# Kernel optimization log

Measured on AMD Instinct MI355X. Metric: run time of the kernel, lower is better.

Reference implementation:

```python
import jax, jax.numpy as jnp
import numpy as np

NEG_INF = -1e12
BN_EPS = 1e-5
ALPHA = 0.2  # LeakyReLU negative slope


def setup_inputs() -> dict:
    key = jax.random.key(0)
    k1, k2, k3, k4 = jax.random.split(key, 4)
    N, Fin, Fout = 8192, 128, 64
    inp = jax.random.normal(k1, (N, Fin), dtype=jnp.float32)
    adj = jax.random.randint(k2, (N, N), 0, 2, dtype=jnp.int32)
    W = jax.random.normal(k3, (Fin, Fout), dtype=jnp.float32) * (1.414 / np.sqrt(Fin))
    a = jax.random.normal(k4, (2 * Fout, 1), dtype=jnp.float32) * 0.1
    bn_gamma = jnp.ones((Fout,), dtype=jnp.float32)
    bn_beta = jnp.zeros((Fout,), dtype=jnp.float32)
    bn_mean = jnp.zeros((Fout,), dtype=jnp.float32)
    bn_var = jnp.ones((Fout,), dtype=jnp.float32)
    return {"inp": inp, "adj": adj, "W": W, "a": a,
            "bn_gamma": bn_gamma, "bn_beta": bn_beta,
            "bn_mean": bn_mean, "bn_var": bn_var}


def reference(inp, adj, W, a, bn_gamma, bn_beta, bn_mean, bn_var):
    # h: [N, Fout]
    h = inp @ W
    Fout = h.shape[1]
    # Split 'a' into the two halves acting on h_i and h_j:
    # e_ij = leakyrelu(a1 . h_i + a2 . h_j)  (math-equivalent to the
    # O(N^2 * 2F) repeat/cat construction in the original code)
    a1 = a[:Fout, 0]  # [Fout]
    a2 = a[Fout:, 0]  # [Fout]
    f1 = h @ a1       # [N]
    f2 = h @ a2       # [N]
    e = jax.nn.leaky_relu(f1[:, None] + f2[None, :], negative_slope=ALPHA)  # [N, N]
    e = jnp.where(adj > 0, e, NEG_INF)
    attention = jax.nn.softmax(e, axis=1)  # row-wise softmax over neighbors
    # dropout is identity in eval mode
    h_prime = attention @ h  # [N, Fout]
    # BatchNorm1d in eval mode with running stats
    h_prime = (h_prime - bn_mean) * jax.lax.rsqrt(bn_var + BN_EPS) * bn_gamma + bn_beta
    return jax.nn.elu(h_prime)  # concat=True -> ELU
```

## Files before the change

### kernel.cpp

```cpp
#include <hip/hip_runtime.h>
#include <hip/hip_bf16.h>

#define LRALPHA 0.2f
#define NN 8192
#define FIN 128
#define FOUT 64
#define TI 16
#define TJ 128
#define NT (NN / TJ)

typedef __attribute__((ext_vector_type(4))) float f32x4;
typedef __attribute__((ext_vector_type(8))) short bf16x8;
typedef __attribute__((ext_vector_type(4))) int int4v;

__device__ __forceinline__ void barrier_lgkm() {
  asm volatile("s_waitcnt lgkmcnt(0)\n\ts_barrier" ::: "memory");
}

__global__ __launch_bounds__(256) void prep_kernel(
    const float* __restrict__ inp, const float* __restrict__ Wg,
    const float* __restrict__ ag, float* __restrict__ f1,
    float* __restrict__ f2, unsigned short* __restrict__ hT)
{
  __shared__ alignas(16) float WlT[FOUT][FIN + 4];
  const int t = threadIdx.x;
  for (int i = t; i < FIN * FOUT; i += 256)
    WlT[i & 63][i >> 6] = Wg[i];
  __syncthreads();

  const int lane = t & 63;
  const int row0 = blockIdx.x * 16 + (t >> 6) * 4;

  float h0 = 0.f, h1 = 0.f, h2 = 0.f, h3 = 0.f;
  for (int kk = 0; kk < FIN; kk += 4) {
    f32x4 wv = *(const f32x4*)&WlT[lane][kk];
    f32x4 r0 = *(const f32x4*)&inp[(row0 + 0) * FIN + kk];
    f32x4 r1 = *(const f32x4*)&inp[(row0 + 1) * FIN + kk];
    f32x4 r2 = *(const f32x4*)&inp[(row0 + 2) * FIN + kk];
    f32x4 r3 = *(const f32x4*)&inp[(row0 + 3) * FIN + kk];
    h0 += r0[0]*wv[0] + r0[1]*wv[1] + r0[2]*wv[2] + r0[3]*wv[3];
    h1 += r1[0]*wv[0] + r1[1]*wv[1] + r1[2]*wv[2] + r1[3]*wv[3];
    h2 += r2[0]*wv[0] + r2[1]*wv[1] + r2[2]*wv[2] + r2[3]*wv[3];
    h3 += r3[0]*wv[0] + r3[1]*wv[1] + r3[2]*wv[2] + r3[3]*wv[3];
  }

  const float a1v = ag[lane], a2v = ag[64 + lane];
  float hv[4] = {h0, h1, h2, h3};
#pragma unroll
  for (int rr = 0; rr < 4; ++rr) {
    float c1 = hv[rr] * a1v;
    float c2 = hv[rr] * a2v;
#pragma unroll
    for (int off = 32; off > 0; off >>= 1) {
      c1 += __shfl_xor(c1, off);
      c2 += __shfl_xor(c2, off);
    }
    if (lane == 0) { f1[row0 + rr] = c1; f2[row0 + rr] = c2; }
    __hip_bfloat16 hb = __float2bfloat16(hv[rr]);
    hT[lane * NN + row0 + rr] = __builtin_bit_cast(unsigned short, hb);
  }
}

__global__ __launch_bounds__(256) void f2max_kernel(
    const float* __restrict__ f2, float* __restrict__ f2m)
{
  const int t = threadIdx.x;
  float m = -1e30f;
  for (int i = t; i < NN / 4; i += 256) {
    f32x4 v = ((const f32x4*)f2)[i];
    m = fmaxf(fmaxf(m, fmaxf(v[0], v[1])), fmaxf(v[2], v[3]));
  }
#pragma unroll
  for (int off = 32; off > 0; off >>= 1)
    m = fmaxf(m, __shfl_xor(m, off));
  __shared__ float ms[4];
  if ((t & 63) == 0) ms[t >> 6] = m;
  __syncthreads();
  if (t == 0)
    f2m[0] = fmaxf(fmaxf(ms[0], ms[1]), fmaxf(ms[2], ms[3]));
}

__global__ __launch_bounds__(256, 2) void gat_main(
    const int* __restrict__ adj, const float* __restrict__ f1g,
    const float* __restrict__ f2g, const float* __restrict__ f2m,
    const unsigned short* __restrict__ hTg,
    const float* __restrict__ bng, const float* __restrict__ bnb,
    const float* __restrict__ bnm, const float* __restrict__ bnv,
    float* __restrict__ out)
{
  __shared__ alignas(16) unsigned short Pl[TI][TJ + 8];
  __shared__ alignas(16) unsigned short Hl[FOUT][TJ + 8];

  const int t = threadIdx.x;
  const int i0 = blockIdx.x * TI;

  const int pr = t >> 4;
  const int pj = (t & 15) << 3;

  const float f1v = f1g[i0 + pr];
  const float fmv = f2m[0];
  float mrow = f1v + fmv;
  mrow = mrow > 0.f ? mrow : LRALPHA * mrow;

  const int hc = t >> 2;
  const int hj = (t & 3) << 5;

  const int* adjrow = adj + (i0 + pr) * NN + pj;
  const unsigned short* hrow = hTg + hc * NN + hj;
  const float* f2row = f2g + pj;

  f32x4 acc  = {0.f, 0.f, 0.f, 0.f};
  f32x4 accs = {0.f, 0.f, 0.f, 0.f};

  const short ob = (short)0x3F80;
  const bf16x8 onesv = {ob, ob, ob, ob, ob, ob, ob, ob};

  int4v aA0 = __builtin_nontemporal_load((const int4v*)adjrow);
  int4v aA1 = __builtin_nontemporal_load((const int4v*)(adjrow + 4));
  f32x4 fA0 = *(const f32x4*)f2row;
  f32x4 fA1 = *(const f32x4*)(f2row + 4);
  int4v hA0 = *(const int4v*)hrow;
  int4v hA1 = *(const int4v*)(hrow + 8);
  int4v hA2 = *(const int4v*)(hrow + 16);
  int4v hA3 = *(const int4v*)(hrow + 24);

  int4v aB0 = __builtin_nontemporal_load((const int4v*)(adjrow + TJ));
  int4v aB1 = __builtin_nontemporal_load((const int4v*)(adjrow + TJ + 4));
  f32x4 fB0 = *(const f32x4*)(f2row + TJ);
  f32x4 fB1 = *(const f32x4*)(f2row + TJ + 4);
  int4v hB0 = *(const int4v*)(hrow + TJ);
  int4v hB1 = *(const int4v*)(hrow + TJ + 8);
  int4v hB2 = *(const int4v*)(hrow + TJ + 16);
  int4v hB3 = *(const int4v*)(hrow + TJ + 24);

  const int l = t & 63;
  const int w = t >> 6;
  const int koff = (l >> 4) << 3;
  const unsigned short* pA = &Pl[l & 15][koff];
  const unsigned short* pB = &Hl[(w << 4) + (l & 15)][koff];

#define TILE_BODY(TT, AJ0, AJ1, F20, F21, H0, H1, H2, H3)                      \
  {                                                                            \
    float x0 = f1v + F20[0]; x0 = (x0 > 0.f ? x0 : LRALPHA * x0) - mrow;       \
    float x1 = f1v + F20[1]; x1 = (x1 > 0.f ? x1 : LRALPHA * x1) - mrow;       \
    float x2 = f1v + F20[2]; x2 = (x2 > 0.f ? x2 : LRALPHA * x2) - mrow;       \
    float x3 = f1v + F20[3]; x3 = (x3 > 0.f ? x3 : LRALPHA * x3) - mrow;       \
    float x4 = f1v + F21[0]; x4 = (x4 > 0.f ? x4 : LRALPHA * x4) - mrow;       \
    float x5 = f1v + F21[1]; x5 = (x5 > 0.f ? x5 : LRALPHA * x5) - mrow;       \
    float x6 = f1v + F21[2]; x6 = (x6 > 0.f ? x6 : LRALPHA * x6) - mrow;       \
    float x7 = f1v + F21[3]; x7 = (x7 > 0.f ? x7 : LRALPHA * x7) - mrow;       \
    float p0 = AJ0[0] > 0 ? __expf(x0) : 0.f;                                  \
    float p1 = AJ0[1] > 0 ? __expf(x1) : 0.f;                                  \
    float p2 = AJ0[2] > 0 ? __expf(x2) : 0.f;                                  \
    float p3 = AJ0[3] > 0 ? __expf(x3) : 0.f;                                  \
    float p4 = AJ1[0] > 0 ? __expf(x4) : 0.f;                                  \
    float p5 = AJ1[1] > 0 ? __expf(x5) : 0.f;                                  \
    float p6 = AJ1[2] > 0 ? __expf(x6) : 0.f;                                  \
    float p7 = AJ1[3] > 0 ? __expf(x7) : 0.f;                                  \
    unsigned short u0 = __builtin_bit_cast(unsigned short, __float2bfloat16(p0)); \
    unsigned short u1 = __builtin_bit_cast(unsigned short, __float2bfloat16(p1)); \
    unsigned short u2 = __builtin_bit_cast(unsigned short, __float2bfloat16(p2)); \
    unsigned short u3 = __builtin_bit_cast(unsigned short, __float2bfloat16(p3)); \
    unsigned short u4 = __builtin_bit_cast(unsigned short, __float2bfloat16(p4)); \
    unsigned short u5 = __builtin_bit_cast(unsigned short, __float2bfloat16(p5)); \
    unsigned short u6 = __builtin_bit_cast(unsigned short, __float2bfloat16(p6)); \
    unsigned short u7 = __builtin_bit_cast(unsigned short, __float2bfloat16(p7)); \
    int4v pw = {(int)u0 | ((int)u1 << 16), (int)u2 | ((int)u3 << 16),          \
                (int)u4 | ((int)u5 << 16), (int)u6 | ((int)u7 << 16)};         \
    *(int4v*)&Pl[pr][pj] = pw;                                                 \
    *(int4v*)&Hl[hc][hj]      = H0;                                            \
    *(int4v*)&Hl[hc][hj + 8]  = H1;                                            \
    *(int4v*)&Hl[hc][hj + 16] = H2;                                            \
    *(int4v*)&Hl[hc][hj + 24] = H3;                                            \
    if ((TT) + 2 < NT) {                                                       \
      AJ0 = __builtin_nontemporal_load((const int4v*)(adjrow + ((TT)+2)*TJ));      \
      AJ1 = __builtin_nontemporal_load((const int4v*)(adjrow + ((TT)+2)*TJ + 4));  \
      F20 = *(const f32x4*)(f2row + ((TT)+2)*TJ);                              \
      F21 = *(const f32x4*)(f2row + ((TT)+2)*TJ + 4);                          \
      H0 = *(const int4v*)(hrow + ((TT)+2)*TJ);                                \
      H1 = *(const int4v*)(hrow + ((TT)+2)*TJ + 8);                            \
      H2 = *(const int4v*)(hrow + ((TT)+2)*TJ + 16);                           \
      H3 = *(const int4v*)(hrow + ((TT)+2)*TJ + 24);                           \
    }                                                                          \
    barrier_lgkm();                                                            \
    {                                                                          \
      bf16x8 av, bv;                                                           \
      av = *(const bf16x8*)(pA);       bv = *(const bf16x8*)(pB);              \
      acc  = __builtin_amdgcn_mfma_f32_16x16x32_bf16(av, bv, acc, 0, 0, 0);    \
      accs = __builtin_amdgcn_mfma_f32_16x16x32_bf16(av, onesv, accs, 0, 0, 0);\
      av = *(const bf16x8*)(pA + 32);  bv = *(const bf16x8*)(pB + 32);         \
      acc  = __builtin_amdgcn_mfma_f32_16x16x32_bf16(av, bv, acc, 0, 0, 0);    \
      accs = __builtin_amdgcn_mfma_f32_16x16x32_bf16(av, onesv, accs, 0, 0, 0);\
      av = *(const bf16x8*)(pA + 64);  bv = *(const bf16x8*)(pB + 64);         \
      acc  = __builtin_amdgcn_mfma_f32_16x16x32_bf16(av, bv, acc, 0, 0, 0);    \
      accs = __builtin_amdgcn_mfma_f32_16x16x32_bf16(av, onesv, accs, 0, 0, 0);\
      av = *(const bf16x8*)(pA + 96);  bv = *(const bf16x8*)(pB + 96);         \
      acc  = __builtin_amdgcn_mfma_f32_16x16x32_bf16(av, bv, acc, 0, 0, 0);    \
      accs = __builtin_amdgcn_mfma_f32_16x16x32_bf16(av, onesv, accs, 0, 0, 0);\
    }                                                                          \
    barrier_lgkm();                                                            \
  }

  for (int tt = 0; tt < NT; tt += 2) {
    TILE_BODY(tt,     aA0, aA1, fA0, fA1, hA0, hA1, hA2, hA3);
    TILE_BODY(tt + 1, aB0, aB1, fB0, fB1, hB0, hB1, hB2, hB3);
  }
#undef TILE_BODY

  const int gcol = (w << 4) + (l & 15);
  const float inv_sd = rsqrtf(bnv[gcol] + 1e-5f);
  const float ga = bng[gcol], be = bnb[gcol], mu = bnm[gcol];
  const int rbase = (l >> 4) << 2;
#pragma unroll
  for (int q = 0; q < 4; ++q) {
    float v = acc[q] / accs[q];
    v = (v - mu) * inv_sd * ga + be;
    v = v > 0.f ? v : expm1f(v);
    out[(i0 + rbase + q) * FOUT + gcol] = v;
  }
}

extern "C" void kernel_launch(void* const* d_in, const int* in_sizes, int n_in,
                              void* d_out, int out_size, void* d_ws, size_t ws_size,
                              hipStream_t stream)
{
  (void)in_sizes; (void)n_in; (void)out_size; (void)ws_size;
  const float* inp = (const float*)d_in[0];
  const int*   adj = (const int*)d_in[1];
  const float* Wg  = (const float*)d_in[2];
  const float* ag  = (const float*)d_in[3];
  const float* bng = (const float*)d_in[4];
  const float* bnb = (const float*)d_in[5];
  const float* bnm = (const float*)d_in[6];
  const float* bnv = (const float*)d_in[7];
  float* out = (float*)d_out;

  char* ws = (char*)d_ws;
  unsigned short* hT = (unsigned short*)ws;
  float* f1 = (float*)(ws + (size_t)NN * FOUT * 2);
  float* f2 = f1 + NN;
  float* f2m = f2 + NN;

  prep_kernel<<<NN / 16, 256, 0, stream>>>(inp, Wg, ag, f1, f2, hT);
  f2max_kernel<<<1, 256, 0, stream>>>(f2, f2m);
  gat_main<<<NN / TI, 256, 0, stream>>>(adj, f1, f2, f2m, hT,
                                        bng, bnb, bnm, bnv, out);
}
```

Measured before the change: 105.3 us.

## Deepen prefetch to four tiles and compute softmax row sums in fp32

Raises the register prefetch depth from two to four tiles of adjacency, f2 and hT data, to hide more global-memory latency. Drops the extra MFMA that multiplied P by a ones vector to get the denominator. Each thread now accumulates the row sum in fp32 and reduces it with shuffles and shared memory. Adjacency loads are split into two 16-byte halves at offsets 0 and 64, and LeakyReLU uses fmaxf. The deeper prefetch costs more VGPRs, which may hurt occupancy under launch_bounds(256,2), and past the end it reloads the last tile redundantly.

```diff
diff --git a/kernel.cpp b/kernel.cpp
--- a/kernel.cpp
+++ b/kernel.cpp
@@ -12,6 +12,7 @@
 typedef __attribute__((ext_vector_type(4))) float f32x4;
 typedef __attribute__((ext_vector_type(8))) short bf16x8;
 typedef __attribute__((ext_vector_type(4))) int int4v;
+typedef __attribute__((ext_vector_type(2))) int int2v;
 
 __device__ __forceinline__ void barrier_lgkm() {
   asm volatile("s_waitcnt lgkmcnt(0)\n\ts_barrier" ::: "memory");
@@ -90,12 +91,13 @@
 {
   __shared__ alignas(16) unsigned short Pl[TI][TJ + 8];
   __shared__ alignas(16) unsigned short Hl[FOUT][TJ + 8];
+  __shared__ float rs_lds[TI];
 
   const int t = threadIdx.x;
   const int i0 = blockIdx.x * TI;
 
   const int pr = t >> 4;
-  const int pj = (t & 15) << 3;
+  const int c  = t & 15;
 
   const float f1v = f1g[i0 + pr];
   const float fmv = f2m[0];
@@ -105,33 +107,12 @@
   const int hc = t >> 2;
   const int hj = (t & 3) << 5;
 
-  const int* adjrow = adj + (i0 + pr) * NN + pj;
+  const int* adjrow = adj + (i0 + pr) * NN + c * 4;
   const unsigned short* hrow = hTg + hc * NN + hj;
-  const float* f2row = f2g + pj;
-
-  f32x4 acc  = {0.f, 0.f, 0.f, 0.f};
-  f32x4 accs = {0.f, 0.f, 0.f, 0.f};
-
-  const short ob = (short)0x3F80;
-  const bf16x8 onesv = {ob, ob, ob, ob, ob, ob, ob, ob};
-
-  int4v aA0 = __builtin_nontemporal_load((const int4v*)adjrow);
-  int4v aA1 = __builtin_nontemporal_load((const int4v*)(adjrow + 4));
-  f32x4 fA0 = *(const f32x4*)f2row;
-  f32x4 fA1 = *(const f32x4*)(f2row + 4);
-  int4v hA0 = *(const int4v*)hrow;
-  int4v hA1 = *(const int4v*)(hrow + 8);
-  int4v hA2 = *(const int4v*)(hrow + 16);
-  int4v hA3 = *(const int4v*)(hrow + 24);
-
-  int4v aB0 = __builtin_nontemporal_load((const int4v*)(adjrow + TJ));
-  int4v aB1 = __builtin_nontemporal_load((const int4v*)(adjrow + TJ + 4));
-  f32x4 fB0 = *(const f32x4*)(f2row + TJ);
-  f32x4 fB1 = *(const f32x4*)(f2row + TJ + 4);
-  int4v hB0 = *(const int4v*)(hrow + TJ);
-  int4v hB1 = *(const int4v*)(hrow + TJ + 8);
-  int4v hB2 = *(const int4v*)(hrow + TJ + 16);
-  int4v hB3 = *(const int4v*)(hrow + TJ + 24);
+  const float* f2row = f2g + c * 4;
+
+  f32x4 acc = {0.f, 0.f, 0.f, 0.f};
+  float rs = 0.f;
 
   const int l = t & 63;
   const int w = t >> 6;
@@ -139,24 +120,48 @@
   const unsigned short* pA = &Pl[l & 15][koff];
   const unsigned short* pB = &Hl[(w << 4) + (l & 15)][koff];
 
-#define TILE_BODY(TT, AJ0, AJ1, F20, F21, H0, H1, H2, H3)                      \
+  int4v aA0,aA1,aB0,aB1,aC0,aC1,aD0,aD1;
+  f32x4 fA0,fA1,fB0,fB1,fC0,fC1,fD0,fD1;
+  int4v hA0,hA1,hA2,hA3,hB0,hB1,hB2,hB3;
+  int4v hC0,hC1,hC2,hC3,hD0,hD1,hD2,hD3;
+
+#define PREF(A0,A1,F0,F1,H0,H1,H2,H3,T)                                        \
   {                                                                            \
-    float x0 = f1v + F20[0]; x0 = (x0 > 0.f ? x0 : LRALPHA * x0) - mrow;       \
-    float x1 = f1v + F20[1]; x1 = (x1 > 0.f ? x1 : LRALPHA * x1) - mrow;       \
-    float x2 = f1v + F20[2]; x2 = (x2 > 0.f ? x2 : LRALPHA * x2) - mrow;       \
-    float x3 = f1v + F20[3]; x3 = (x3 > 0.f ? x3 : LRALPHA * x3) - mrow;       \
-    float x4 = f1v + F21[0]; x4 = (x4 > 0.f ? x4 : LRALPHA * x4) - mrow;       \
-    float x5 = f1v + F21[1]; x5 = (x5 > 0.f ? x5 : LRALPHA * x5) - mrow;       \
-    float x6 = f1v + F21[2]; x6 = (x6 > 0.f ? x6 : LRALPHA * x6) - mrow;       \
-    float x7 = f1v + F21[3]; x7 = (x7 > 0.f ? x7 : LRALPHA * x7) - mrow;       \
-    float p0 = AJ0[0] > 0 ? __expf(x0) : 0.f;                                  \
-    float p1 = AJ0[1] > 0 ? __expf(x1) : 0.f;                                  \
-    float p2 = AJ0[2] > 0 ? __expf(x2) : 0.f;                                  \
-    float p3 = AJ0[3] > 0 ? __expf(x3) : 0.f;                                  \
-    float p4 = AJ1[0] > 0 ? __expf(x4) : 0.f;                                  \
-    float p5 = AJ1[1] > 0 ? __expf(x5) : 0.f;                                  \
-    float p6 = AJ1[2] > 0 ? __expf(x6) : 0.f;                                  \
-    float p7 = AJ1[3] > 0 ? __expf(x7) : 0.f;                                  \
+    const int _tn = (T) < NT ? (T) : (NT - 1);                                 \
+    A0 = __builtin_nontemporal_load((const int4v*)(adjrow + _tn * TJ));        \
+    A1 = __builtin_nontemporal_load((const int4v*)(adjrow + _tn * TJ + 64));   \
+    F0 = *(const f32x4*)(f2row + _tn * TJ);                                    \
+    F1 = *(const f32x4*)(f2row + _tn * TJ + 64);                               \
+    H0 = *(const int4v*)(hrow + _tn * TJ);                                     \
+    H1 = *(const int4v*)(hrow + _tn * TJ + 8);                                 \
+    H2 = *(const int4v*)(hrow + _tn * TJ + 16);                                \
+    H3 = *(const int4v*)(hrow + _tn * TJ + 24);                                \
+  }
+
+  PREF(aA0,aA1,fA0,fA1,hA0,hA1,hA2,hA3, 0);
+  PREF(aB0,aB1,fB0,fB1,hB0,hB1,hB2,hB3, 1);
+  PREF(aC0,aC1,fC0,fC1,hC0,hC1,hC2,hC3, 2);
+  PREF(aD0,aD1,fD0,fD1,hD0,hD1,hD2,hD3, 3);
+
+#define TILE_BODY(A0,A1,F0,F1,H0,H1,H2,H3,T)                                   \
+  {                                                                            \
+    float x0 = f1v + F0[0]; x0 = fmaxf(x0, LRALPHA * x0) - mrow;               \
+    float x1 = f1v + F0[1]; x1 = fmaxf(x1, LRALPHA * x1) - mrow;               \
+    float x2 = f1v + F0[2]; x2 = fmaxf(x2, LRALPHA * x2) - mrow;               \
+    float x3 = f1v + F0[3]; x3 = fmaxf(x3, LRALPHA * x3) - mrow;               \
+    float x4 = f1v + F1[0]; x4 = fmaxf(x4, LRALPHA * x4) - mrow;               \
+    float x5 = f1v + F1[1]; x5 = fmaxf(x5, LRALPHA * x5) - mrow;               \
+    float x6 = f1v + F1[2]; x6 = fmaxf(x6, LRALPHA * x6) - mrow;               \
+    float x7 = f1v + F1[3]; x7 = fmaxf(x7, LRALPHA * x7) - mrow;               \
+    float p0 = A0[0] > 0 ? __expf(x0) : 0.f;                                   \
+    float p1 = A0[1] > 0 ? __expf(x1) : 0.f;                                   \
+    float p2 = A0[2] > 0 ? __expf(x2) : 0.f;                                   \
+    float p3 = A0[3] > 0 ? __expf(x3) : 0.f;                                   \
+    float p4 = A1[0] > 0 ? __expf(x4) : 0.f;                                   \
+    float p5 = A1[1] > 0 ? __expf(x5) : 0.f;                                   \
+    float p6 = A1[2] > 0 ? __expf(x6) : 0.f;                                   \
+    float p7 = A1[3] > 0 ? __expf(x7) : 0.f;                                   \
+    rs += ((p0 + p1) + (p2 + p3)) + ((p4 + p5) + (p6 + p7));                   \
     unsigned short u0 = __builtin_bit_cast(unsigned short, __float2bfloat16(p0)); \
     unsigned short u1 = __builtin_bit_cast(unsigned short, __float2bfloat16(p1)); \
     unsigned short u2 = __builtin_bit_cast(unsigned short, __float2bfloat16(p2)); \
@@ -165,47 +170,45 @@
     unsigned short u5 = __builtin_bit_cast(unsigned short, __float2bfloat16(p5)); \
     unsigned short u6 = __builtin_bit_cast(unsigned short, __float2bfloat16(p6)); \
     unsigned short u7 = __builtin_bit_cast(unsigned short, __float2bfloat16(p7)); \
-    int4v pw = {(int)u0 | ((int)u1 << 16), (int)u2 | ((int)u3 << 16),          \
-                (int)u4 | ((int)u5 << 16), (int)u6 | ((int)u7 << 16)};         \
-    *(int4v*)&Pl[pr][pj] = pw;                                                 \
+    int2v pw0 = {(int)u0 | ((int)u1 << 16), (int)u2 | ((int)u3 << 16)};        \
+    int2v pw1 = {(int)u4 | ((int)u5 << 16), (int)u6 | ((int)u7 << 16)};        \
+    *(int2v*)&Pl[pr][c * 4]      = pw0;                                        \
+    *(int2v*)&Pl[pr][64 + c * 4] = pw1;                                        \
     *(int4v*)&Hl[hc][hj]      = H0;                                            \
     *(int4v*)&Hl[hc][hj + 8]  = H1;                                            \
     *(int4v*)&Hl[hc][hj + 16] = H2;                                            \
     *(int4v*)&Hl[hc][hj + 24] = H3;                                            \
-    if ((TT) + 2 < NT) {                                                       \
-      AJ0 = __builtin_nontemporal_load((const int4v*)(adjrow + ((TT)+2)*TJ));      \
-      AJ1 = __builtin_nontemporal_load((const int4v*)(adjrow + ((TT)+2)*TJ + 4));  \
-      F20 = *(const f32x4*)(f2row + ((TT)+2)*TJ);                              \
-      F21 = *(const f32x4*)(f2row + ((TT)+2)*TJ + 4);                          \
-      H0 = *(const int4v*)(hrow + ((TT)+2)*TJ);                                \
-      H1 = *(const int4v*)(hrow + ((TT)+2)*TJ + 8);                            \
-      H2 = *(const int4v*)(hrow + ((TT)+2)*TJ + 16);                           \
-      H3 = *(const int4v*)(hrow + ((TT)+2)*TJ + 24);                           \
-    }                                                                          \
+    PREF(A0,A1,F0,F1,H0,H1,H2,H3, (T) + 4);                                    \
     barrier_lgkm();                                                            \
     {                                                                          \
       bf16x8 av, bv;                                                           \
       av = *(const bf16x8*)(pA);       bv = *(const bf16x8*)(pB);              \
-      acc  = __builtin_amdgcn_mfma_f32_16x16x32_bf16(av, bv, acc, 0, 0, 0);    \
-      accs = __builtin_amdgcn_mfma_f32_16x16x32_bf16(av, onesv, accs, 0, 0, 0);\
+      acc = __builtin_amdgcn_mfma_f32_16x16x32_bf16(av, bv, acc, 0, 0, 0);     \
       av = *(const bf16x8*)(pA + 32);  bv = *(const bf16x8*)(pB + 32);         \
-      acc  = __builtin_amdgcn_mfma_f32_16x16x32_bf16(av, bv, acc, 0, 0, 0);    \
-      accs = __builtin_amdgcn_mfma_f32_16x16x32_bf16(av, onesv, accs, 0, 0, 0);\
+      acc = __builtin_amdgcn_mfma_f32_16x16x32_bf16(av, bv, acc, 0, 0, 0);     \
       av = *(const bf16x8*)(pA + 64);  bv = *(const bf16x8*)(pB + 64);         \
-      acc  = __builtin_amdgcn_mfma_f32_16x16x32_bf16(av, bv, acc, 0, 0, 0);    \
-      accs = __builtin_amdgcn_mfma_f32_16x16x32_bf16(av, onesv, accs, 0, 0, 0);\
+      acc = __builtin_amdgcn_mfma_f32_16x16x32_bf16(av, bv, acc, 0, 0, 0);     \
       av = *(const bf16x8*)(pA + 96);  bv = *(const bf16x8*)(pB + 96);         \
-      acc  = __builtin_amdgcn_mfma_f32_16x16x32_bf16(av, bv, acc, 0, 0, 0);    \
-      accs = __builtin_amdgcn_mfma_f32_16x16x32_bf16(av, onesv, accs, 0, 0, 0);\
+      acc = __builtin_amdgcn_mfma_f32_16x16x32_bf16(av, bv, acc, 0, 0, 0);     \
     }                                                                          \
     barrier_lgkm();                                                            \
   }
 
-  for (int tt = 0; tt < NT; tt += 2) {
-    TILE_BODY(tt,     aA0, aA1, fA0, fA1, hA0, hA1, hA2, hA3);
-    TILE_BODY(tt + 1, aB0, aB1, fB0, fB1, hB0, hB1, hB2, hB3);
+  for (int tt = 0; tt < NT; tt += 4) {
+    TILE_BODY(aA0,aA1,fA0,fA1,hA0,hA1,hA2,hA3, tt);
+    TILE_BODY(aB0,aB1,fB0,fB1,hB0,hB1,hB2,hB3, tt + 1);
+    TILE_BODY(aC0,aC1,fC0,fC1,hC0,hC1,hC2,hC3, tt + 2);
+    TILE_BODY(aD0,aD1,fD0,fD1,hD0,hD1,hD2,hD3, tt + 3);
   }
 #undef TILE_BODY
+#undef PREF
+
+  rs += __shfl_xor(rs, 1);
+  rs += __shfl_xor(rs, 2);
+  rs += __shfl_xor(rs, 4);
+  rs += __shfl_xor(rs, 8);
+  if (c == 0) rs_lds[pr] = rs;
+  __syncthreads();
 
   const int gcol = (w << 4) + (l & 15);
   const float inv_sd = rsqrtf(bnv[gcol] + 1e-5f);
@@ -213,7 +216,7 @@
   const int rbase = (l >> 4) << 2;
 #pragma unroll
   for (int q = 0; q < 4; ++q) {
-    float v = acc[q] / accs[q];
+    float v = acc[q] / rs_lds[rbase + q];
     v = (v - mu) * inv_sd * ga + be;
     v = v > 0.f ? v : expm1f(v);
     out[(i0 + rbase + q) * FOUT + gcol] = v;
```

After: 104.5 us. No clear change (-0.8%).
